# Kernel tuning notes

Measured on AMD Instinct MI355X. Metric: run time of the kernel, lower is better.

Reference implementation:

```python
import jax, jax.numpy as jnp
import numpy as np

B, I, H, O = 16384, 512, 1024, 512

def setup_inputs() -> dict:
    key = jax.random.key(0)
    ks = jax.random.split(key, 8)
    s_x = 1.0 / np.sqrt(I)
    s_h = 1.0 / np.sqrt(H)
    inp = jax.random.normal(ks[0], (B, I), jnp.float32)
    h = jax.random.normal(ks[1], (B, H), jnp.float32)
    c = jax.random.normal(ks[2], (B, H), jnp.float32)
    # stacked gate weights, order [i, o, f, z]
    Wx = jax.random.uniform(ks[3], (4, H, I), jnp.float32, -s_x, s_x)
    Wh = jax.random.uniform(ks[4], (4, H, H), jnp.float32, -s_h, s_h)
    # z-gate h2z weight is re-initialized with standard normal in reset_parameters
    Wh = Wh.at[3].set(jax.random.normal(ks[5], (H, H), jnp.float32))
    # biases per module init: i=linspace(-1,-10), o=0, f=linspace(1,10), z=0
    bx = jnp.stack([
        jnp.linspace(-1.0, -10.0, H, dtype=jnp.float32),
        jnp.zeros((H,), jnp.float32),
        jnp.linspace(1.0, 10.0, H, dtype=jnp.float32),
        jnp.zeros((H,), jnp.float32),
    ])
    Wout = jax.random.uniform(ks[6], (O, H), jnp.float32, -s_h, s_h)
    bout = jax.random.uniform(ks[7], (O,), jnp.float32, -s_h, s_h)
    return {"inp": inp, "h": h, "c": c, "Wx": Wx, "bx": bx, "Wh": Wh,
            "Wout": Wout, "bout": bout}

def reference(inp, h, c, Wx, bx, Wh, Wout, bout):
    # fused gate pre-activations: two stacked GEMMs
    # gx: [4, B, H], gh: [4, B, H]
    gx = jnp.einsum('bi,ghi->gbh', inp, Wx) + bx[:, None, :]
    gh = jnp.einsum('bh,gkh->gbk', h, Wh)
    g = gx + gh
    i = jax.nn.sigmoid(g[0])
    o = jax.nn.sigmoid(g[1])
    f = jax.nn.sigmoid(g[2])
    z = jnp.tanh(g[3])
    c_new = i * z + f * c
    h_new = o * jnp.tanh(c_new)  # act_fn = tanh
    out = h_new @ Wout.T + bout
    return (out, h_new)
```

## Files before the change

kernel.cpp:

```cpp
#include <hip/hip_runtime.h>
#include <stdint.h>

#define BB 16384
#define II 512
#define HH 1024
#define OO 512
#define KK1 1536
#define NN1 4096

typedef short s16x8 __attribute__((ext_vector_type(8)));
typedef float f32x4 __attribute__((ext_vector_type(4)));

__device__ __forceinline__ unsigned short f2bf(float x) {
  union { float f; unsigned u; } v; v.f = x;
  return (unsigned short)((v.u + 0x7fffu + ((v.u >> 16) & 1u)) >> 16);
}
__device__ __forceinline__ float bf2f(unsigned short b) {
  union { unsigned u; float f; } v; v.u = ((unsigned)b) << 16;
  return v.f;
}
__device__ __forceinline__ float sigmoid_f(float x) {
  return 1.0f / (1.0f + __expf(-x));
}
__device__ __forceinline__ float tanh_f(float x) {
  float ax = fabsf(x);
  float e = __expf(-2.0f * ax);
  float t = (1.0f - e) / (1.0f + e);
  return x >= 0.0f ? t : -t;
}

__device__ __forceinline__ void stage16(const void* g, void* l) {
  __builtin_amdgcn_global_load_lds((const __attribute__((address_space(1))) void*)g,
                                   (__attribute__((address_space(3))) void*)l,
                                   16, 0, 0);
}

__device__ __forceinline__ void mma_step(const unsigned short* As, const unsigned short* Bs,
                                         f32x4 acc[4][4], int lane, int wave) {
  const int wm = wave & 1, wn = wave >> 1;
  const int ln = lane & 15, q = lane >> 4;
  s16x8 af[4], bfr[4];
#pragma unroll
  for (int i = 0; i < 4; ++i)
    af[i] = *(const s16x8*)(As + (wm * 64 + i * 16 + ln) * 32 + q * 8);
#pragma unroll
  for (int i = 0; i < 4; ++i)
    bfr[i] = *(const s16x8*)(Bs + (wn * 64 + i * 16 + ln) * 32 + q * 8);
#pragma unroll
  for (int mi = 0; mi < 4; ++mi)
#pragma unroll
    for (int ni = 0; ni < 4; ++ni)
      acc[mi][ni] = __builtin_amdgcn_mfma_f32_16x16x32_bf16(af[mi], bfr[ni], acc[mi][ni], 0, 0, 0);
}


__global__ __launch_bounds__(256) void prep_X(const float* __restrict__ inp,
                                              const float* __restrict__ h,
                                              unsigned short* __restrict__ Xb,
                                              unsigned short* __restrict__ Hlo) {
  int t = blockIdx.x * 256 + threadIdx.x;
  int base = t * 8;
  int b = base / 1536;
  int k = base - b * 1536;
  const float* src = (k < 512) ? (inp + b * 512 + k) : (h + b * 1024 + (k - 512));
  float4 v0 = *(const float4*)src;
  float4 v1 = *(const float4*)(src + 4);
  float f[8] = {v0.x, v0.y, v0.z, v0.w, v1.x, v1.y, v1.z, v1.w};
  unsigned short hi[8];
#pragma unroll
  for (int i = 0; i < 8; ++i) hi[i] = f2bf(f[i]);
  *(s16x8*)(Xb + base) = *(s16x8*)hi;
  if (k >= 512) {
    unsigned short lo[8];
#pragma unroll
    for (int i = 0; i < 8; ++i) lo[i] = f2bf(f[i] - bf2f(hi[i]));
    *(s16x8*)(Hlo + b * 1024 + (k - 512)) = *(s16x8*)lo;
  }
}

__global__ __launch_bounds__(256) void prep_Wg(const float* __restrict__ Wx,
                                               const float* __restrict__ Wh,
                                               unsigned short* __restrict__ Wg) {
  int t = blockIdx.x * 256 + threadIdx.x;
  int base = t * 8;
  int n = base / 1536;
  int k = base - n * 1536;
  int r = n & 127;
  int gate = (r >> 4) & 3;
  int unit = ((n >> 7) << 5) + (((r >> 6) & 1) << 4) + (r & 15);
  const float* src = (k < 512) ? (Wx + (gate * 1024 + unit) * 512 + k)
                               : (Wh + (gate * 1024 + unit) * 1024 + (k - 512));
  float4 v0 = *(const float4*)src;
  float4 v1 = *(const float4*)(src + 4);
  float f[8] = {v0.x, v0.y, v0.z, v0.w, v1.x, v1.y, v1.z, v1.w};
  unsigned short o[8];
#pragma unroll
  for (int i = 0; i < 8; ++i) o[i] = f2bf(f[i]);
  *(s16x8*)(Wg + base) = *(s16x8*)o;
}

__global__ __launch_bounds__(256) void prep_Wz2(const float* __restrict__ Whz,
                                                unsigned short* __restrict__ Wz2) {
  int t = blockIdx.x * 256 + threadIdx.x;
  int base = t * 8;
  int n = base >> 11;
  int k = base & 2047;
  int klo = (k < 1024) ? k : (k - 1024);
  const float* src = Whz + n * 1024 + klo;
  float4 v0 = *(const float4*)src;
  float4 v1 = *(const float4*)(src + 4);
  float f[8] = {v0.x, v0.y, v0.z, v0.w, v1.x, v1.y, v1.z, v1.w};
  unsigned short o[8];
  if (k < 1024) {
#pragma unroll
    for (int i = 0; i < 8; ++i) { unsigned short h_ = f2bf(f[i]); o[i] = f2bf(f[i] - bf2f(h_)); }
  } else {
#pragma unroll
    for (int i = 0; i < 8; ++i) o[i] = f2bf(f[i]);
  }
  *(s16x8*)(Wz2 + base) = *(s16x8*)o;
}

__global__ __launch_bounds__(256) void prep_Wout(const float* __restrict__ Wout,
                                                 unsigned short* __restrict__ Wo) {
  int t = blockIdx.x * 256 + threadIdx.x;
  int base = t * 8;
  float4 v0 = *(const float4*)(Wout + base);
  float4 v1 = *(const float4*)(Wout + base + 4);
  float f[8] = {v0.x, v0.y, v0.z, v0.w, v1.x, v1.y, v1.z, v1.w};
  unsigned short o[8];
#pragma unroll
  for (int i = 0; i < 8; ++i) o[i] = f2bf(f[i]);
  *(s16x8*)(Wo + base) = *(s16x8*)o;
}


__global__ __launch_bounds__(256) void gemm_zcorr(const unsigned short* __restrict__ Xb,
                                                  const unsigned short* __restrict__ Hlo,
                                                  const unsigned short* __restrict__ Wz2,
                                                  unsigned short* __restrict__ Dgz) {
  __shared__ unsigned short As[4096];
  __shared__ unsigned short Bs[4096];
  const int n0 = blockIdx.x * 128;
  const int m0 = blockIdx.y * 128;
  const int tid = threadIdx.x, lane = tid & 63, wave = tid >> 6;
  const int c0 = wave * 64 + lane, c1 = c0 + 256;
  const int r0 = c0 >> 2, kc0 = (c0 & 3) << 3;
  const int r1 = c1 >> 2, kc1 = (c1 & 3) << 3;
  unsigned short* la0 = As + wave * 512;
  unsigned short* la1 = As + 2048 + wave * 512;
  unsigned short* lb0 = Bs + wave * 512;
  unsigned short* lb1 = Bs + 2048 + wave * 512;
  const unsigned short* gb0 = Wz2 + (n0 + r0) * 2048 + kc0;
  const unsigned short* gb1 = Wz2 + (n0 + r1) * 2048 + kc1;
  const int rowA0 = m0 + r0, rowA1 = m0 + r1;
  f32x4 acc[4][4] = {};
  for (int kk = 0; kk < 64; ++kk) {
    const int k0 = kk * 32;
    const unsigned short *ga0, *ga1;
    if (k0 < 1024) {
      ga0 = Xb + rowA0 * 1536 + 512 + k0 + kc0;
      ga1 = Xb + rowA1 * 1536 + 512 + k0 + kc1;
    } else {
      ga0 = Hlo + rowA0 * 1024 + (k0 - 1024) + kc0;
      ga1 = Hlo + rowA1 * 1024 + (k0 - 1024) + kc1;
    }
    stage16(ga0, la0); stage16(ga1, la1);
    stage16(gb0, lb0); stage16(gb1, lb1);
    gb0 += 32; gb1 += 32;
    __syncthreads();
    mma_step(As, Bs, acc, lane, wave);
    __syncthreads();
  }
  const int wm = wave & 1, wn = wave >> 1;
  const int ln = lane & 15, q = lane >> 4;
#pragma unroll
  for (int mi = 0; mi < 4; ++mi) {
#pragma unroll
    for (int r = 0; r < 4; ++r) {
      const int b = m0 + wm * 64 + mi * 16 + q * 4 + r;
#pragma unroll
      for (int ni = 0; ni < 4; ++ni) {
        const int n = n0 + wn * 64 + ni * 16 + ln;
        Dgz[b * 1024 + n] = f2bf(acc[mi][ni][r]);
      }
    }
  }
}

__global__ __launch_bounds__(256) void gemm_gates(const unsigned short* __restrict__ Xb,
                                                   const unsigned short* __restrict__ Wg,
                                                   const float* __restrict__ bx,
                                                   const float* __restrict__ cold,
                                                   const unsigned short* __restrict__ Dgz,
                                                   float* __restrict__ hnew,
                                                   unsigned short* __restrict__ hnewb) {
  __shared__ unsigned short As[4096];
  __shared__ unsigned short Bs[4096];
  const int n0 = blockIdx.x * 128;
  const int m0 = blockIdx.y * 128;
  const int tid = threadIdx.x, lane = tid & 63, wave = tid >> 6;
  const int c0 = wave * 64 + lane, c1 = c0 + 256;
  const int r0 = c0 >> 2, kc0 = (c0 & 3) << 3;
  const int r1 = c1 >> 2, kc1 = (c1 & 3) << 3;
  unsigned short* la0 = As + wave * 512;
  unsigned short* la1 = As + 2048 + wave * 512;
  unsigned short* lb0 = Bs + wave * 512;
  unsigned short* lb1 = Bs + 2048 + wave * 512;
  const unsigned short* ga0 = Xb + (m0 + r0) * 1536 + kc0;
  const unsigned short* ga1 = Xb + (m0 + r1) * 1536 + kc1;
  const unsigned short* gb0 = Wg + (n0 + r0) * 1536 + kc0;
  const unsigned short* gb1 = Wg + (n0 + r1) * 1536 + kc1;
  f32x4 acc[4][4] = {};
  for (int kk = 0; kk < 48; ++kk) {
    stage16(ga0, la0); stage16(ga1, la1);
    stage16(gb0, lb0); stage16(gb1, lb1);
    ga0 += 32; ga1 += 32; gb0 += 32; gb1 += 32;
    __syncthreads();
    mma_step(As, Bs, acc, lane, wave);
    __syncthreads();
  }
  const int wm = wave & 1, wn = wave >> 1;
  const int ln = lane & 15, q = lane >> 4;
  const int unit = (blockIdx.x << 5) + (wn << 4) + ln;
  const float bi = bx[unit];
  const float bo = bx[1024 + unit];
  const float bfg = bx[2048 + unit];
  const float bz = bx[3072 + unit];
#pragma unroll
  for (int mi = 0; mi < 4; ++mi) {
#pragma unroll
    for (int r = 0; r < 4; ++r) {
      const int b = m0 + wm * 64 + mi * 16 + q * 4 + r;
      const int idx = b * 1024 + unit;
      const float gi = acc[mi][0][r] + bi;
      const float go = acc[mi][1][r] + bo;
      const float gf = acc[mi][2][r] + bfg;
      const float gz = acc[mi][3][r] + bz + bf2f(Dgz[idx]);
      const float iv = sigmoid_f(gi);
      const float ov = sigmoid_f(go);
      const float fv = sigmoid_f(gf);
      const float zv = tanh_f(gz);
      const float cn = iv * zv + fv * cold[idx];
      const float hn = ov * tanh_f(cn);
      hnew[idx] = hn;
      hnewb[idx] = f2bf(hn);
    }
  }
}

__global__ __launch_bounds__(256) void gemm_out(const unsigned short* __restrict__ Hb,
                                                const unsigned short* __restrict__ Wo,
                                                const float* __restrict__ bout,
                                                float* __restrict__ out) {
  __shared__ unsigned short As[4096];
  __shared__ unsigned short Bs[4096];
  const int n0 = blockIdx.x * 128;
  const int m0 = blockIdx.y * 128;
  const int tid = threadIdx.x, lane = tid & 63, wave = tid >> 6;
  const int c0 = wave * 64 + lane, c1 = c0 + 256;
  const int r0 = c0 >> 2, kc0 = (c0 & 3) << 3;
  const int r1 = c1 >> 2, kc1 = (c1 & 3) << 3;
  unsigned short* la0 = As + wave * 512;
  unsigned short* la1 = As + 2048 + wave * 512;
  unsigned short* lb0 = Bs + wave * 512;
  unsigned short* lb1 = Bs + 2048 + wave * 512;
  const unsigned short* ga0 = Hb + (m0 + r0) * 1024 + kc0;
  const unsigned short* ga1 = Hb + (m0 + r1) * 1024 + kc1;
  const unsigned short* gb0 = Wo + (n0 + r0) * 1024 + kc0;
  const unsigned short* gb1 = Wo + (n0 + r1) * 1024 + kc1;
  f32x4 acc[4][4] = {};
  for (int kk = 0; kk < 32; ++kk) {
    stage16(ga0, la0); stage16(ga1, la1);
    stage16(gb0, lb0); stage16(gb1, lb1);
    ga0 += 32; ga1 += 32; gb0 += 32; gb1 += 32;
    __syncthreads();
    mma_step(As, Bs, acc, lane, wave);
    __syncthreads();
  }
  const int wm = wave & 1, wn = wave >> 1;
  const int ln = lane & 15, q = lane >> 4;
  float bo_[4];
#pragma unroll
  for (int ni = 0; ni < 4; ++ni) bo_[ni] = bout[n0 + wn * 64 + ni * 16 + ln];
#pragma unroll
  for (int mi = 0; mi < 4; ++mi) {
#pragma unroll
    for (int r = 0; r < 4; ++r) {
      const int b = m0 + wm * 64 + mi * 16 + q * 4 + r;
#pragma unroll
      for (int ni = 0; ni < 4; ++ni) {
        const int n = n0 + wn * 64 + ni * 16 + ln;
        out[b * 512 + n] = acc[mi][ni][r] + bo_[ni];
      }
    }
  }
}

extern "C" void kernel_launch(void* const* d_in, const int* in_sizes, int n_in,
                              void* d_out, int out_size, void* d_ws, size_t ws_size,
                              hipStream_t stream) {
  const float* inp  = (const float*)d_in[0];
  const float* h    = (const float*)d_in[1];
  const float* c    = (const float*)d_in[2];
  const float* Wx   = (const float*)d_in[3];
  const float* bx   = (const float*)d_in[4];
  const float* Wh   = (const float*)d_in[5];
  const float* Wout = (const float*)d_in[6];
  const float* bout = (const float*)d_in[7];

  float* out  = (float*)d_out;
  float* hnew = out + (size_t)BB * OO;

  char* ws = (char*)d_ws;
  unsigned short* Xb  = (unsigned short*)(ws);
  unsigned short* Wg  = (unsigned short*)(ws + 50331648);
  unsigned short* Wo  = (unsigned short*)(ws + 62914560);
  unsigned short* Hb  = (unsigned short*)(ws + 63963136);
  unsigned short* Hlo = (unsigned short*)(ws + 97517568);
  unsigned short* Wz2 = (unsigned short*)(ws + 131072000);
  unsigned short* Dgz = (unsigned short*)(ws + 135266304);

  prep_X   <<<12288, 256, 0, stream>>>(inp, h, Xb, Hlo);
  prep_Wg  <<<3072,  256, 0, stream>>>(Wx, Wh, Wg);
  prep_Wz2 <<<1024,  256, 0, stream>>>(Wh + 3 * 1024 * 1024, Wz2);
  prep_Wout<<<256,   256, 0, stream>>>(Wout, Wo);
  gemm_zcorr<<<dim3(8, 128),  256, 0, stream>>>(Xb, Hlo, Wz2, Dgz);
  gemm_gates<<<dim3(32, 128), 256, 0, stream>>>(Xb, Wg, bx, c, Dgz, hnew, Hb);
  gemm_out  <<<dim3(4, 128),  256, 0, stream>>>(Hb, Wo, bout, out);
}
```

Baseline: 670.0 us.

## Double K-tile depth to 64 and XOR-swizzle LDS layout in all GEMMs

Each GEMM kernel now stages a 128x64 K-slice per iteration instead of 128x32, halving the number of barrier pairs per output tile. The LDS layout uses a rotation swizzle of 16-byte chunks, applied on the global source side so the direct global-to-LDS loads stay contiguous per wave while the MFMA fragment reads avoid bank conflicts. The zcorr kernel also drops the per-iteration branch between X and Hlo by splitting its loop in two. LDS use per block doubles, which may reduce occupancy.

```diff
diff --git a/kernel.cpp b/kernel.cpp
--- a/kernel.cpp
+++ b/kernel.cpp
@@ -5,8 +5,6 @@
 #define II 512
 #define HH 1024
 #define OO 512
-#define KK1 1536
-#define NN1 4096
 
 typedef short s16x8 __attribute__((ext_vector_type(8)));
 typedef float f32x4 __attribute__((ext_vector_type(4)));
@@ -35,22 +33,29 @@
                                    16, 0, 0);
 }
 
-__device__ __forceinline__ void mma_step(const unsigned short* As, const unsigned short* Bs,
-                                         f32x4 acc[4][4], int lane, int wave) {
+__device__ __forceinline__ void mma_step64(const unsigned short* As, const unsigned short* Bs,
+                                           f32x4 acc[4][4], int lane, int wave) {
   const int wm = wave & 1, wn = wave >> 1;
   const int ln = lane & 15, q = lane >> 4;
-  s16x8 af[4], bfr[4];
-#pragma unroll
-  for (int i = 0; i < 4; ++i)
-    af[i] = *(const s16x8*)(As + (wm * 64 + i * 16 + ln) * 32 + q * 8);
-#pragma unroll
-  for (int i = 0; i < 4; ++i)
-    bfr[i] = *(const s16x8*)(Bs + (wn * 64 + i * 16 + ln) * 32 + q * 8);
-#pragma unroll
-  for (int mi = 0; mi < 4; ++mi)
-#pragma unroll
-    for (int ni = 0; ni < 4; ++ni)
-      acc[mi][ni] = __builtin_amdgcn_mfma_f32_16x16x32_bf16(af[mi], bfr[ni], acc[mi][ni], 0, 0, 0);
+#pragma unroll
+  for (int s = 0; s < 2; ++s) {
+    s16x8 af[4], bfr[4];
+#pragma unroll
+    for (int i = 0; i < 4; ++i) {
+      const int r = wm * 64 + i * 16 + ln;
+      af[i] = *(const s16x8*)(As + r * 64 + ((((s << 2) + q) + r) & 7) * 8);
+    }
+#pragma unroll
+    for (int i = 0; i < 4; ++i) {
+      const int r = wn * 64 + i * 16 + ln;
+      bfr[i] = *(const s16x8*)(Bs + r * 64 + ((((s << 2) + q) + r) & 7) * 8);
+    }
+#pragma unroll
+    for (int mi = 0; mi < 4; ++mi)
+#pragma unroll
+      for (int ni = 0; ni < 4; ++ni)
+        acc[mi][ni] = __builtin_amdgcn_mfma_f32_16x16x32_bf16(af[mi], bfr[ni], acc[mi][ni], 0, 0, 0);
+  }
 }
 
 
@@ -139,37 +144,41 @@
                                                   const unsigned short* __restrict__ Hlo,
                                                   const unsigned short* __restrict__ Wz2,
                                                   unsigned short* __restrict__ Dgz) {
-  __shared__ unsigned short As[4096];
-  __shared__ unsigned short Bs[4096];
+  __shared__ unsigned short As[8192];
+  __shared__ unsigned short Bs[8192];
   const int n0 = blockIdx.x * 128;
   const int m0 = blockIdx.y * 128;
   const int tid = threadIdx.x, lane = tid & 63, wave = tid >> 6;
-  const int c0 = wave * 64 + lane, c1 = c0 + 256;
-  const int r0 = c0 >> 2, kc0 = (c0 & 3) << 3;
-  const int r1 = c1 >> 2, kc1 = (c1 & 3) << 3;
-  unsigned short* la0 = As + wave * 512;
-  unsigned short* la1 = As + 2048 + wave * 512;
-  unsigned short* lb0 = Bs + wave * 512;
-  unsigned short* lb1 = Bs + 2048 + wave * 512;
-  const unsigned short* gb0 = Wz2 + (n0 + r0) * 2048 + kc0;
-  const unsigned short* gb1 = Wz2 + (n0 + r1) * 2048 + kc1;
-  const int rowA0 = m0 + r0, rowA1 = m0 + r1;
+  const unsigned short *gaX[4], *gaH[4], *gb[4];
+  unsigned short *la[4], *lb[4];
+#pragma unroll
+  for (int u = 0; u < 4; ++u) {
+    int p = u * 256 + tid;
+    int r = p >> 3;
+    int j = ((p & 7) - r) & 7;
+    gaX[u] = Xb + (size_t)(m0 + r) * 1536 + 512 + j * 8;
+    gaH[u] = Hlo + (size_t)(m0 + r) * 1024 + j * 8;
+    gb[u]  = Wz2 + (size_t)(n0 + r) * 2048 + j * 8;
+    la[u] = As + (u * 256 + (tid & ~63)) * 8;
+    lb[u] = Bs + (u * 256 + (tid & ~63)) * 8;
+  }
   f32x4 acc[4][4] = {};
-  for (int kk = 0; kk < 64; ++kk) {
-    const int k0 = kk * 32;
-    const unsigned short *ga0, *ga1;
-    if (k0 < 1024) {
-      ga0 = Xb + rowA0 * 1536 + 512 + k0 + kc0;
-      ga1 = Xb + rowA1 * 1536 + 512 + k0 + kc1;
-    } else {
-      ga0 = Hlo + rowA0 * 1024 + (k0 - 1024) + kc0;
-      ga1 = Hlo + rowA1 * 1024 + (k0 - 1024) + kc1;
-    }
-    stage16(ga0, la0); stage16(ga1, la1);
-    stage16(gb0, lb0); stage16(gb1, lb1);
-    gb0 += 32; gb1 += 32;
-    __syncthreads();
-    mma_step(As, Bs, acc, lane, wave);
+  for (int kk = 0; kk < 16; ++kk) {
+#pragma unroll
+    for (int u = 0; u < 4; ++u) { stage16(gaX[u], la[u]); stage16(gb[u], lb[u]); }
+#pragma unroll
+    for (int u = 0; u < 4; ++u) { gaX[u] += 64; gb[u] += 64; }
+    __syncthreads();
+    mma_step64(As, Bs, acc, lane, wave);
+    __syncthreads();
+  }
+  for (int kk = 0; kk < 16; ++kk) {
+#pragma unroll
+    for (int u = 0; u < 4; ++u) { stage16(gaH[u], la[u]); stage16(gb[u], lb[u]); }
+#pragma unroll
+    for (int u = 0; u < 4; ++u) { gaH[u] += 64; gb[u] += 64; }
+    __syncthreads();
+    mma_step64(As, Bs, acc, lane, wave);
     __syncthreads();
   }
   const int wm = wave & 1, wn = wave >> 1;
@@ -195,29 +204,31 @@
                                                    const unsigned short* __restrict__ Dgz,
                                                    float* __restrict__ hnew,
                                                    unsigned short* __restrict__ hnewb) {
-  __shared__ unsigned short As[4096];
-  __shared__ unsigned short Bs[4096];
+  __shared__ unsigned short As[8192];
+  __shared__ unsigned short Bs[8192];
   const int n0 = blockIdx.x * 128;
   const int m0 = blockIdx.y * 128;
   const int tid = threadIdx.x, lane = tid & 63, wave = tid >> 6;
-  const int c0 = wave * 64 + lane, c1 = c0 + 256;
-  const int r0 = c0 >> 2, kc0 = (c0 & 3) << 3;
-  const int r1 = c1 >> 2, kc1 = (c1 & 3) << 3;
-  unsigned short* la0 = As + wave * 512;
-  unsigned short* la1 = As + 2048 + wave * 512;
-  unsigned short* lb0 = Bs + wave * 512;
-  unsigned short* lb1 = Bs + 2048 + wave * 512;
-  const unsigned short* ga0 = Xb + (m0 + r0) * 1536 + kc0;
-  const unsigned short* ga1 = Xb + (m0 + r1) * 1536 + kc1;
-  const unsigned short* gb0 = Wg + (n0 + r0) * 1536 + kc0;
-  const unsigned short* gb1 = Wg + (n0 + r1) * 1536 + kc1;
+  const unsigned short *ga[4], *gb[4];
+  unsigned short *la[4], *lb[4];
+#pragma unroll
+  for (int u = 0; u < 4; ++u) {
+    int p = u * 256 + tid;
+    int r = p >> 3;
+    int j = ((p & 7) - r) & 7;
+    ga[u] = Xb + (size_t)(m0 + r) * 1536 + j * 8;
+    gb[u] = Wg + (size_t)(n0 + r) * 1536 + j * 8;
+    la[u] = As + (u * 256 + (tid & ~63)) * 8;
+    lb[u] = Bs + (u * 256 + (tid & ~63)) * 8;
+  }
   f32x4 acc[4][4] = {};
-  for (int kk = 0; kk < 48; ++kk) {
-    stage16(ga0, la0); stage16(ga1, la1);
-    stage16(gb0, lb0); stage16(gb1, lb1);
-    ga0 += 32; ga1 += 32; gb0 += 32; gb1 += 32;
-    __syncthreads();
-    mma_step(As, Bs, acc, lane, wave);
+  for (int kk = 0; kk < 24; ++kk) {
+#pragma unroll
+    for (int u = 0; u < 4; ++u) { stage16(ga[u], la[u]); stage16(gb[u], lb[u]); }
+#pragma unroll
+    for (int u = 0; u < 4; ++u) { ga[u] += 64; gb[u] += 64; }
+    __syncthreads();
+    mma_step64(As, Bs, acc, lane, wave);
     __syncthreads();
   }
   const int wm = wave & 1, wn = wave >> 1;
@@ -253,29 +264,31 @@
                                                 const unsigned short* __restrict__ Wo,
                                                 const float* __restrict__ bout,
                                                 float* __restrict__ out) {
-  __shared__ unsigned short As[4096];
-  __shared__ unsigned short Bs[4096];
+  __shared__ unsigned short As[8192];
+  __shared__ unsigned short Bs[8192];
   const int n0 = blockIdx.x * 128;
   const int m0 = blockIdx.y * 128;
   const int tid = threadIdx.x, lane = tid & 63, wave = tid >> 6;
-  const int c0 = wave * 64 + lane, c1 = c0 + 256;
-  const int r0 = c0 >> 2, kc0 = (c0 & 3) << 3;
-  const int r1 = c1 >> 2, kc1 = (c1 & 3) << 3;
-  unsigned short* la0 = As + wave * 512;
-  unsigned short* la1 = As + 2048 + wave * 512;
-  unsigned short* lb0 = Bs + wave * 512;
-  unsigned short* lb1 = Bs + 2048 + wave * 512;
-  const unsigned short* ga0 = Hb + (m0 + r0) * 1024 + kc0;
-  const unsigned short* ga1 = Hb + (m0 + r1) * 1024 + kc1;
-  const unsigned short* gb0 = Wo + (n0 + r0) * 1024 + kc0;
-  const unsigned short* gb1 = Wo + (n0 + r1) * 1024 + kc1;
+  const unsigned short *ga[4], *gb[4];
+  unsigned short *la[4], *lb[4];
+#pragma unroll
+  for (int u = 0; u < 4; ++u) {
+    int p = u * 256 + tid;
+    int r = p >> 3;
+    int j = ((p & 7) - r) & 7;
+    ga[u] = Hb + (size_t)(m0 + r) * 1024 + j * 8;
+    gb[u] = Wo + (size_t)(n0 + r) * 1024 + j * 8;
+    la[u] = As + (u * 256 + (tid & ~63)) * 8;
+    lb[u] = Bs + (u * 256 + (tid & ~63)) * 8;
+  }
   f32x4 acc[4][4] = {};
-  for (int kk = 0; kk < 32; ++kk) {
-    stage16(ga0, la0); stage16(ga1, la1);
-    stage16(gb0, lb0); stage16(gb1, lb1);
-    ga0 += 32; ga1 += 32; gb0 += 32; gb1 += 32;
-    __syncthreads();
-    mma_step(As, Bs, acc, lane, wave);
+  for (int kk = 0; kk < 16; ++kk) {
+#pragma unroll
+    for (int u = 0; u < 4; ++u) { stage16(ga[u], la[u]); stage16(gb[u], lb[u]); }
+#pragma unroll
+    for (int u = 0; u < 4; ++u) { ga[u] += 64; gb[u] += 64; }
+    __syncthreads();
+    mma_step64(As, Bs, acc, lane, wave);
     __syncthreads();
   }
   const int wm = wave & 1, wn = wave >> 1;
```

Result: faster. 632.4 us (-5.6%).

## Double-buffer GEMM LDS tiles with swizzled layout and merge prep kernels

Applied to the files above, without the earlier changes.

All three GEMMs now use double-buffered LDS. The loads for the next K tile are issued before the current tile's MFMAs, so only one barrier is needed per iteration instead of two. The LDS layout is XOR/rotate-swizzled per row to reduce bank conflicts on the fragment reads. The four conversion kernels are merged into one launch to cut launch overhead. The cost is twice the LDS per block, which may lower occupancy.

```diff
diff --git a/kernel.cpp b/kernel.cpp
--- a/kernel.cpp
+++ b/kernel.cpp
@@ -5,8 +5,6 @@
 #define II 512
 #define HH 1024
 #define OO 512
-#define KK1 1536
-#define NN1 4096
 
 typedef short s16x8 __attribute__((ext_vector_type(8)));
 typedef float f32x4 __attribute__((ext_vector_type(4)));
@@ -35,158 +33,125 @@
                                    16, 0, 0);
 }
 
-__device__ __forceinline__ void mma_step(const unsigned short* As, const unsigned short* Bs,
-                                         f32x4 acc[4][4], int lane, int wave) {
-  const int wm = wave & 1, wn = wave >> 1;
-  const int ln = lane & 15, q = lane >> 4;
-  s16x8 af[4], bfr[4];
-#pragma unroll
-  for (int i = 0; i < 4; ++i)
-    af[i] = *(const s16x8*)(As + (wm * 64 + i * 16 + ln) * 32 + q * 8);
-#pragma unroll
-  for (int i = 0; i < 4; ++i)
-    bfr[i] = *(const s16x8*)(Bs + (wn * 64 + i * 16 + ln) * 32 + q * 8);
-#pragma unroll
-  for (int mi = 0; mi < 4; ++mi)
-#pragma unroll
-    for (int ni = 0; ni < 4; ++ni)
-      acc[mi][ni] = __builtin_amdgcn_mfma_f32_16x16x32_bf16(af[mi], bfr[ni], acc[mi][ni], 0, 0, 0);
-}
-
-
-__global__ __launch_bounds__(256) void prep_X(const float* __restrict__ inp,
-                                              const float* __restrict__ h,
-                                              unsigned short* __restrict__ Xb,
-                                              unsigned short* __restrict__ Hlo) {
-  int t = blockIdx.x * 256 + threadIdx.x;
-  int base = t * 8;
-  int b = base / 1536;
-  int k = base - b * 1536;
-  const float* src = (k < 512) ? (inp + b * 512 + k) : (h + b * 1024 + (k - 512));
-  float4 v0 = *(const float4*)src;
-  float4 v1 = *(const float4*)(src + 4);
-  float f[8] = {v0.x, v0.y, v0.z, v0.w, v1.x, v1.y, v1.z, v1.w};
-  unsigned short hi[8];
-#pragma unroll
-  for (int i = 0; i < 8; ++i) hi[i] = f2bf(f[i]);
-  *(s16x8*)(Xb + base) = *(s16x8*)hi;
-  if (k >= 512) {
-    unsigned short lo[8];
-#pragma unroll
-    for (int i = 0; i < 8; ++i) lo[i] = f2bf(f[i] - bf2f(hi[i]));
-    *(s16x8*)(Hlo + b * 1024 + (k - 512)) = *(s16x8*)lo;
-  }
-}
-
-__global__ __launch_bounds__(256) void prep_Wg(const float* __restrict__ Wx,
-                                               const float* __restrict__ Wh,
-                                               unsigned short* __restrict__ Wg) {
-  int t = blockIdx.x * 256 + threadIdx.x;
-  int base = t * 8;
-  int n = base / 1536;
-  int k = base - n * 1536;
-  int r = n & 127;
-  int gate = (r >> 4) & 3;
-  int unit = ((n >> 7) << 5) + (((r >> 6) & 1) << 4) + (r & 15);
-  const float* src = (k < 512) ? (Wx + (gate * 1024 + unit) * 512 + k)
-                               : (Wh + (gate * 1024 + unit) * 1024 + (k - 512));
-  float4 v0 = *(const float4*)src;
-  float4 v1 = *(const float4*)(src + 4);
-  float f[8] = {v0.x, v0.y, v0.z, v0.w, v1.x, v1.y, v1.z, v1.w};
-  unsigned short o[8];
-#pragma unroll
-  for (int i = 0; i < 8; ++i) o[i] = f2bf(f[i]);
-  *(s16x8*)(Wg + base) = *(s16x8*)o;
-}
-
-__global__ __launch_bounds__(256) void prep_Wz2(const float* __restrict__ Whz,
-                                                unsigned short* __restrict__ Wz2) {
-  int t = blockIdx.x * 256 + threadIdx.x;
-  int base = t * 8;
-  int n = base >> 11;
-  int k = base & 2047;
-  int klo = (k < 1024) ? k : (k - 1024);
-  const float* src = Whz + n * 1024 + klo;
-  float4 v0 = *(const float4*)src;
-  float4 v1 = *(const float4*)(src + 4);
-  float f[8] = {v0.x, v0.y, v0.z, v0.w, v1.x, v1.y, v1.z, v1.w};
-  unsigned short o[8];
-  if (k < 1024) {
-#pragma unroll
-    for (int i = 0; i < 8; ++i) { unsigned short h_ = f2bf(f[i]); o[i] = f2bf(f[i] - bf2f(h_)); }
+__global__ __launch_bounds__(256) void prep_all(const float* __restrict__ inp,
+                                                const float* __restrict__ h,
+                                                const float* __restrict__ Wx,
+                                                const float* __restrict__ Wh,
+                                                const float* __restrict__ Wout,
+                                                unsigned short* __restrict__ Xb,
+                                                unsigned short* __restrict__ Hlo,
+                                                unsigned short* __restrict__ Wg,
+                                                unsigned short* __restrict__ Wz2,
+                                                unsigned short* __restrict__ Wo) {
+  const int bid = blockIdx.x;
+  if (bid < 12288) {
+    int t = bid * 256 + threadIdx.x;
+    int base = t * 8;
+    int b = base / 1536;
+    int k = base - b * 1536;
+    const float* src = (k < 512) ? (inp + b * 512 + k) : (h + b * 1024 + (k - 512));
+    float4 v0 = *(const float4*)src;
+    float4 v1 = *(const float4*)(src + 4);
+    float f[8] = {v0.x, v0.y, v0.z, v0.w, v1.x, v1.y, v1.z, v1.w};
+    unsigned short hi[8];
+#pragma unroll
+    for (int i = 0; i < 8; ++i) hi[i] = f2bf(f[i]);
+    *(s16x8*)(Xb + base) = *(s16x8*)hi;
+    if (k >= 512) {
+      unsigned short lo[8];
+#pragma unroll
+      for (int i = 0; i < 8; ++i) lo[i] = f2bf(f[i] - bf2f(hi[i]));
+      *(s16x8*)(Hlo + b * 1024 + (k - 512)) = *(s16x8*)lo;
+    }
+  } else if (bid < 15360) {
+    int t = (bid - 12288) * 256 + threadIdx.x;
+    int base = t * 8;
+    int n = base / 1536;
+    int k = base - n * 1536;
+    int r = n & 127;
+    int gate = (r >> 4) & 3;
+    int unit = ((n >> 7) << 5) + (((r >> 6) & 1) << 4) + (r & 15);
+    const float* src = (k < 512) ? (Wx + (gate * 1024 + unit) * 512 + k)
+                                 : (Wh + (gate * 1024 + unit) * 1024 + (k - 512));
+    float4 v0 = *(const float4*)src;
+    float4 v1 = *(const float4*)(src + 4);
+    float f[8] = {v0.x, v0.y, v0.z, v0.w, v1.x, v1.y, v1.z, v1.w};
+    unsigned short o[8];
+#pragma unroll
+    for (int i = 0; i < 8; ++i) o[i] = f2bf(f[i]);
+    *(s16x8*)(Wg + base) = *(s16x8*)o;
+  } else if (bid < 16384) {
+    int t = (bid - 15360) * 256 + threadIdx.x;
+    int base = t * 8;
+    int n = base >> 11;
+    int k = base & 2047;
+    int klo = (k < 1024) ? k : (k - 1024);
+    const float* src = Wh + (size_t)3 * 1024 * 1024 + n * 1024 + klo;
+    float4 v0 = *(const float4*)src;
+    float4 v1 = *(const float4*)(src + 4);
+    float f[8] = {v0.x, v0.y, v0.z, v0.w, v1.x, v1.y, v1.z, v1.w};
+    unsigned short o[8];
+    if (k < 1024) {
+#pragma unroll
+      for (int i = 0; i < 8; ++i) { unsigned short h_ = f2bf(f[i]); o[i] = f2bf(f[i] - bf2f(h_)); }
+    } else {
+#pragma unroll
+      for (int i = 0; i < 8; ++i) o[i] = f2bf(f[i]);
+    }
+    *(s16x8*)(Wz2 + base) = *(s16x8*)o;
   } else {
+    int t = (bid - 16384) * 256 + threadIdx.x;
+    int base = t * 8;
+    float4 v0 = *(const float4*)(Wout + base);
+    float4 v1 = *(const float4*)(Wout + base + 4);
+    float f[8] = {v0.x, v0.y, v0.z, v0.w, v1.x, v1.y, v1.z, v1.w};
+    unsigned short o[8];
 #pragma unroll
     for (int i = 0; i < 8; ++i) o[i] = f2bf(f[i]);
-  }
-  *(s16x8*)(Wz2 + base) = *(s16x8*)o;
-}
-
-__global__ __launch_bounds__(256) void prep_Wout(const float* __restrict__ Wout,
-                                                 unsigned short* __restrict__ Wo) {
-  int t = blockIdx.x * 256 + threadIdx.x;
-  int base = t * 8;
-  float4 v0 = *(const float4*)(Wout + base);
-  float4 v1 = *(const float4*)(Wout + base + 4);
-  float f[8] = {v0.x, v0.y, v0.z, v0.w, v1.x, v1.y, v1.z, v1.w};
-  unsigned short o[8];
-#pragma unroll
-  for (int i = 0; i < 8; ++i) o[i] = f2bf(f[i]);
-  *(s16x8*)(Wo + base) = *(s16x8*)o;
-}
-
-
-__global__ __launch_bounds__(256) void gemm_zcorr(const unsigned short* __restrict__ Xb,
-                                                  const unsigned short* __restrict__ Hlo,
-                                                  const unsigned short* __restrict__ Wz2,
-                                                  unsigned short* __restrict__ Dgz) {
-  __shared__ unsigned short As[4096];
-  __shared__ unsigned short Bs[4096];
-  const int n0 = blockIdx.x * 128;
-  const int m0 = blockIdx.y * 128;
-  const int tid = threadIdx.x, lane = tid & 63, wave = tid >> 6;
-  const int c0 = wave * 64 + lane, c1 = c0 + 256;
-  const int r0 = c0 >> 2, kc0 = (c0 & 3) << 3;
-  const int r1 = c1 >> 2, kc1 = (c1 & 3) << 3;
-  unsigned short* la0 = As + wave * 512;
-  unsigned short* la1 = As + 2048 + wave * 512;
-  unsigned short* lb0 = Bs + wave * 512;
-  unsigned short* lb1 = Bs + 2048 + wave * 512;
-  const unsigned short* gb0 = Wz2 + (n0 + r0) * 2048 + kc0;
-  const unsigned short* gb1 = Wz2 + (n0 + r1) * 2048 + kc1;
-  const int rowA0 = m0 + r0, rowA1 = m0 + r1;
+    *(s16x8*)(Wo + base) = *(s16x8*)o;
+  }
+}
+
+
+#define GEMM_PROLOGUE(APTR, ALD, BPTR, BLD)                                  \
+  __shared__ unsigned short As[8192];                                        \
+  __shared__ unsigned short Bs[8192];                                        \
+  const int tid = threadIdx.x, lane = tid & 63, wave = tid >> 6;             \
+  const unsigned short *ga[2], *gb[2];                                       \
+  unsigned short *laA[2], *laB[2];                                           \
+  _Pragma("unroll")                                                          \
+  for (int t = 0; t < 2; ++t) {                                              \
+    int p = t * 256 + tid;                                                   \
+    int r = p >> 2, c = p & 3, j = (c - r) & 3;                              \
+    ga[t] = (APTR) + (size_t)(m0 + r) * (ALD) + j * 8;                       \
+    gb[t] = (BPTR) + (size_t)(n0 + r) * (BLD) + j * 8;                       \
+    laA[t] = As + (t * 256 + (tid & ~63)) * 8;                               \
+    laB[t] = Bs + (t * 256 + (tid & ~63)) * 8;                               \
+  }                                                                          \
+  const int wm = wave & 1, wn = wave >> 1, ln = lane & 15, q = lane >> 4;    \
+  int aoff[4], boff[4];                                                      \
+  _Pragma("unroll")                                                          \
+  for (int i = 0; i < 4; ++i) {                                              \
+    int ra = wm * 64 + i * 16 + ln; aoff[i] = ra * 32 + (((q + ra) & 3) << 3); \
+    int rb = wn * 64 + i * 16 + ln; boff[i] = rb * 32 + (((q + rb) & 3) << 3); \
+  }                                                                          \
   f32x4 acc[4][4] = {};
-  for (int kk = 0; kk < 64; ++kk) {
-    const int k0 = kk * 32;
-    const unsigned short *ga0, *ga1;
-    if (k0 < 1024) {
-      ga0 = Xb + rowA0 * 1536 + 512 + k0 + kc0;
-      ga1 = Xb + rowA1 * 1536 + 512 + k0 + kc1;
-    } else {
-      ga0 = Hlo + rowA0 * 1024 + (k0 - 1024) + kc0;
-      ga1 = Hlo + rowA1 * 1024 + (k0 - 1024) + kc1;
-    }
-    stage16(ga0, la0); stage16(ga1, la1);
-    stage16(gb0, lb0); stage16(gb1, lb1);
-    gb0 += 32; gb1 += 32;
-    __syncthreads();
-    mma_step(As, Bs, acc, lane, wave);
-    __syncthreads();
-  }
-  const int wm = wave & 1, wn = wave >> 1;
-  const int ln = lane & 15, q = lane >> 4;
-#pragma unroll
-  for (int mi = 0; mi < 4; ++mi) {
-#pragma unroll
-    for (int r = 0; r < 4; ++r) {
-      const int b = m0 + wm * 64 + mi * 16 + q * 4 + r;
-#pragma unroll
-      for (int ni = 0; ni < 4; ++ni) {
-        const int n = n0 + wn * 64 + ni * 16 + ln;
-        Dgz[b * 1024 + n] = f2bf(acc[mi][ni][r]);
-      }
-    }
-  }
-}
+
+#define GEMM_COMPUTE(kk)                                                     \
+  {                                                                          \
+    const unsigned short* A_ = As + ((kk) & 1) * 4096;                       \
+    const unsigned short* B_ = Bs + ((kk) & 1) * 4096;                       \
+    s16x8 af[4], bfr[4];                                                     \
+    _Pragma("unroll")                                                        \
+    for (int i = 0; i < 4; ++i) af[i] = *(const s16x8*)(A_ + aoff[i]);       \
+    _Pragma("unroll")                                                        \
+    for (int i = 0; i < 4; ++i) bfr[i] = *(const s16x8*)(B_ + boff[i]);      \
+    _Pragma("unroll")                                                        \
+    for (int mi = 0; mi < 4; ++mi)                                           \
+      _Pragma("unroll")                                                      \
+      for (int ni = 0; ni < 4; ++ni)                                         \
+        acc[mi][ni] = __builtin_amdgcn_mfma_f32_16x16x32_bf16(af[mi], bfr[ni], acc[mi][ni], 0, 0, 0); \
+  }
 
 __global__ __launch_bounds__(256) void gemm_gates(const unsigned short* __restrict__ Xb,
                                                    const unsigned short* __restrict__ Wg,
@@ -195,33 +160,25 @@
                                                    const unsigned short* __restrict__ Dgz,
                                                    float* __restrict__ hnew,
                                                    unsigned short* __restrict__ hnewb) {
-  __shared__ unsigned short As[4096];
-  __shared__ unsigned short Bs[4096];
   const int n0 = blockIdx.x * 128;
   const int m0 = blockIdx.y * 128;
-  const int tid = threadIdx.x, lane = tid & 63, wave = tid >> 6;
-  const int c0 = wave * 64 + lane, c1 = c0 + 256;
-  const int r0 = c0 >> 2, kc0 = (c0 & 3) << 3;
-  const int r1 = c1 >> 2, kc1 = (c1 & 3) << 3;
-  unsigned short* la0 = As + wave * 512;
-  unsigned short* la1 = As + 2048 + wave * 512;
-  unsigned short* lb0 = Bs + wave * 512;
-  unsigned short* lb1 = Bs + 2048 + wave * 512;
-  const unsigned short* ga0 = Xb + (m0 + r0) * 1536 + kc0;
-  const unsigned short* ga1 = Xb + (m0 + r1) * 1536 + kc1;
-  const unsigned short* gb0 = Wg + (n0 + r0) * 1536 + kc0;
-  const unsigned short* gb1 = Wg + (n0 + r1) * 1536 + kc1;
-  f32x4 acc[4][4] = {};
-  for (int kk = 0; kk < 48; ++kk) {
-    stage16(ga0, la0); stage16(ga1, la1);
-    stage16(gb0, lb0); stage16(gb1, lb1);
-    ga0 += 32; ga1 += 32; gb0 += 32; gb1 += 32;
+  GEMM_PROLOGUE(Xb, 1536, Wg, 1536)
+#pragma unroll
+  for (int t = 0; t < 2; ++t) { stage16(ga[t], laA[t]); stage16(gb[t], laB[t]); }
+  const int NK = 48;
+  for (int kk = 0; kk < NK; ++kk) {
     __syncthreads();
-    mma_step(As, Bs, acc, lane, wave);
-    __syncthreads();
-  }
-  const int wm = wave & 1, wn = wave >> 1;
-  const int ln = lane & 15, q = lane >> 4;
+    if (kk + 1 < NK) {
+      const int ns = ((kk + 1) & 1) * 4096;
+      const int ko = (kk + 1) * 32;
+#pragma unroll
+      for (int t = 0; t < 2; ++t) {
+        stage16(ga[t] + ko, laA[t] + ns);
+        stage16(gb[t] + ko, laB[t] + ns);
+      }
+    }
+    GEMM_COMPUTE(kk)
+  }
   const int unit = (blockIdx.x << 5) + (wn << 4) + ln;
   const float bi = bx[unit];
   const float bo = bx[1024 + unit];
@@ -249,37 +206,75 @@
   }
 }
 
+__global__ __launch_bounds__(256) void gemm_zcorr(const unsigned short* __restrict__ Xb,
+                                                  const unsigned short* __restrict__ Hlo,
+                                                  const unsigned short* __restrict__ Wz2,
+                                                  unsigned short* __restrict__ Dgz) {
+  const int n0 = blockIdx.x * 128;
+  const int m0 = blockIdx.y * 128;
+  GEMM_PROLOGUE(Xb + 512, 1536, Wz2, 2048)
+  const unsigned short* gaH[2];
+#pragma unroll
+  for (int t = 0; t < 2; ++t) {
+    int p = t * 256 + tid;
+    int r = p >> 2, c = p & 3, j = (c - r) & 3;
+    gaH[t] = Hlo + (size_t)(m0 + r) * 1024 + j * 8;
+  }
+#pragma unroll
+  for (int t = 0; t < 2; ++t) { stage16(ga[t], laA[t]); stage16(gb[t], laB[t]); }
+  const int NK = 64;
+  for (int kk = 0; kk < NK; ++kk) {
+    __syncthreads();
+    if (kk + 1 < NK) {
+      const int nt = kk + 1;
+      const int ns = (nt & 1) * 4096;
+#pragma unroll
+      for (int t = 0; t < 2; ++t) {
+        const unsigned short* srcA = (nt < 32) ? (ga[t] + nt * 32)
+                                               : (gaH[t] + (nt - 32) * 32);
+        stage16(srcA, laA[t] + ns);
+        stage16(gb[t] + nt * 32, laB[t] + ns);
+      }
+    }
+    GEMM_COMPUTE(kk)
+  }
+#pragma unroll
+  for (int mi = 0; mi < 4; ++mi) {
+#pragma unroll
+    for (int r = 0; r < 4; ++r) {
+      const int b = m0 + wm * 64 + mi * 16 + q * 4 + r;
+#pragma unroll
+      for (int ni = 0; ni < 4; ++ni) {
+        const int n = n0 + wn * 64 + ni * 16 + ln;
+        Dgz[b * 1024 + n] = f2bf(acc[mi][ni][r]);
+      }
+    }
+  }
+}
+
 __global__ __launch_bounds__(256) void gemm_out(const unsigned short* __restrict__ Hb,
                                                 const unsigned short* __restrict__ Wo,
                                                 const float* __restrict__ bout,
                                                 float* __restrict__ out) {
-  __shared__ unsigned short As[4096];
-  __shared__ unsigned short Bs[4096];
   const int n0 = blockIdx.x * 128;
   const int m0 = blockIdx.y * 128;
-  const int tid = threadIdx.x, lane = tid & 63, wave = tid >> 6;
-  const int c0 = wave * 64 + lane, c1 = c0 + 256;
-  const int r0 = c0 >> 2, kc0 = (c0 & 3) << 3;
-  const int r1 = c1 >> 2, kc1 = (c1 & 3) << 3;
-  unsigned short* la0 = As + wave * 512;
-  unsigned short* la1 = As + 2048 + wave * 512;
-  unsigned short* lb0 = Bs + wave * 512;
-  unsigned short* lb1 = Bs + 2048 + wave * 512;
-  const unsigned short* ga0 = Hb + (m0 + r0) * 1024 + kc0;
-  const unsigned short* ga1 = Hb + (m0 + r1) * 1024 + kc1;
-  const unsigned short* gb0 = Wo + (n0 + r0) * 1024 + kc0;
-  const unsigned short* gb1 = Wo + (n0 + r1) * 1024 + kc1;
-  f32x4 acc[4][4] = {};
-  for (int kk = 0; kk < 32; ++kk) {
-    stage16(ga0, la0); stage16(ga1, la1);
-    stage16(gb0, lb0); stage16(gb1, lb1);
-    ga0 += 32; ga1 += 32; gb0 += 32; gb1 += 32;
+  GEMM_PROLOGUE(Hb, 1024, Wo, 1024)
+#pragma unroll
+  for (int t = 0; t < 2; ++t) { stage16(ga[t], laA[t]); stage16(gb[t], laB[t]); }
+  const int NK = 32;
+  for (int kk = 0; kk < NK; ++kk) {
     __syncthreads();
-    mma_step(As, Bs, acc, lane, wave);
-    __syncthreads();
-  }
-  const int wm = wave & 1, wn = wave >> 1;
-  const int ln = lane & 15, q = lane >> 4;
+    if (kk + 1 < NK) {
+      const int ns = ((kk + 1) & 1) * 4096;
+      const int ko = (kk + 1) * 32;
+#pragma unroll
+      for (int t = 0; t < 2; ++t) {
+        stage16(ga[t] + ko, laA[t] + ns);
+        stage16(gb[t] + ko, laB[t] + ns);
+      }
+    }
+    GEMM_COMPUTE(kk)
+  }
   float bo_[4];
 #pragma unroll
   for (int ni = 0; ni < 4; ++ni) bo_[ni] = bout[n0 + wn * 64 + ni * 16 + ln];
@@ -321,10 +316,7 @@
   unsigned short* Wz2 = (unsigned short*)(ws + 131072000);
   unsigned short* Dgz = (unsigned short*)(ws + 135266304);
 
-  prep_X   <<<12288, 256, 0, stream>>>(inp, h, Xb, Hlo);
-  prep_Wg  <<<3072,  256, 0, stream>>>(Wx, Wh, Wg);
-  prep_Wz2 <<<1024,  256, 0, stream>>>(Wh + 3 * 1024 * 1024, Wz2);
-  prep_Wout<<<256,   256, 0, stream>>>(Wout, Wo);
+  prep_all  <<<16640, 256, 0, stream>>>(inp, h, Wx, Wh, Wout, Xb, Hlo, Wg, Wz2, Wo);
   gemm_zcorr<<<dim3(8, 128),  256, 0, stream>>>(Xb, Hlo, Wz2, Dgz);
   gemm_gates<<<dim3(32, 128), 256, 0, stream>>>(Xb, Wg, bx, c, Dgz, hnew, Hb);
   gemm_out  <<<dim3(4, 128),  256, 0, stream>>>(Hb, Wo, bout, out);
```

Result: slower. 687.8 us (+2.7%).
